# Kernel tuning notes

Hardware: AMD Instinct MI355X
Metric: run time of the kernel (lower is better)

Reference implementation:

```python
import jax, jax.numpy as jnp
import numpy as np

# ---- module hyper-params (match init_kwargs) ----
B, C_IN, C_OUT, K, H, W = 16, 128, 128, 3, 56, 56
M, G, STRIDE, RED = 2, 2, 1, 16
R = max(RED, C_IN // RED)            # GC_Attention bottleneck width = 16
MO = M * C_OUT                       # gc_att output channels
GROUPS = G * C_OUT                   # grouped 1x1 fc groups = 256
IN_PG = MO // GROUPS                 # in channels per group = M // G = 1
COUT_FC = C_OUT * C_IN * K * K       # generated weight elements per sample
OUT_PG = COUT_FC // GROUPS           # out channels per group = 576
PAD = K // 2
LN_EPS = 1e-5


def setup_inputs() -> dict:
    key = jax.random.key(0)
    ks = jax.random.split(key, 6)
    sc = 0.05
    return {
        "x": jax.random.normal(ks[0], (B, C_IN, H, W), jnp.float32),
        # GC_Attention: conv_mask (1x1, C->1)
        "w_mask": jax.random.normal(ks[1], (C_IN,), jnp.float32) * sc,
        "b_mask": jnp.zeros((), jnp.float32),
        # transform: conv1x1 C->R, LayerNorm(R), ReLU, conv1x1 R->M*out
        "w1": jax.random.normal(ks[2], (R, C_IN), jnp.float32) * sc,
        "b1": jnp.zeros((R,), jnp.float32),
        "ln_g": jnp.ones((R,), jnp.float32),
        "ln_b": jnp.zeros((R,), jnp.float32),
        "w2": jax.random.normal(ks[3], (MO, R), jnp.float32) * sc,
        "b2": jnp.zeros((MO,), jnp.float32),
        # fc: grouped 1x1 conv, groups=G*out, stored [groups, out_pg, in_pg]
        "w_fc": jax.random.normal(ks[4], (GROUPS, OUT_PG, IN_PG), jnp.float32) * sc,
        "b_fc": jnp.zeros((COUT_FC,), jnp.float32),
    }


def reference(x, w_mask, b_mask, w1, b1, ln_g, ln_b, w2, b2, w_fc, b_fc):
    b, c, h, w = x.shape
    # --- GC_Attention: global-context pooling via spatial softmax ---
    mask = jnp.einsum('bchw,c->bhw', x, w_mask) + b_mask        # [b,h,w]
    att = jax.nn.softmax(mask.reshape(b, -1), axis=-1)          # [b,hw]
    ctx = jnp.einsum('bcs,bs->bc', x.reshape(b, c, -1), att)    # [b,C]
    # bottleneck transform (1x1 convs on [b,*,1,1] == dense layers)
    t = ctx @ w1.T + b1                                          # [b,R]
    mu = t.mean(-1, keepdims=True)
    var = t.var(-1, keepdims=True)
    t = (t - mu) / jnp.sqrt(var + LN_EPS) * ln_g + ln_b          # LayerNorm over R
    t = jax.nn.relu(t)
    a = jax.nn.sigmoid(t @ w2.T + b2)                            # [b, M*out]
    # --- grouped 1x1 conv: generate per-sample conv weights ---
    xw = jnp.einsum('bgi,goi->bgo', a.reshape(b, GROUPS, IN_PG), w_fc)
    xw = xw.reshape(b, COUT_FC) + b_fc
    Wd = xw.reshape(b, C_OUT, C_IN, K, K)                        # per-sample kernels
    # --- per-sample conv2d (torch: groups=b on batch-folded input) ---
    def conv1(xi, wi):
        return jax.lax.conv_general_dilated(
            xi[None], wi, (STRIDE, STRIDE), [(PAD, PAD), (PAD, PAD)],
            dimension_numbers=('NCHW', 'OIHW', 'NCHW'))[0]
    return jax.vmap(conv1)(x, Wd)                                # [b, out, H, W]
```

## Files before the change

kernel.cpp:

```cpp
#include <hip/hip_runtime.h>
#include <hip/hip_bf16.h>
#include <math.h>

#define BATCH 16
#define CIN   128
#define COUT  128
#define SS    3136
#define XT_ROW 8192
#define XT_PER_B (58*XT_ROW)
#define NKB   18

typedef __attribute__((ext_vector_type(8))) __bf16 bf16x8;
typedef __attribute__((ext_vector_type(4))) float  floatx4;

static __device__ __forceinline__ unsigned short f2bf(float f) {
  union { float f; unsigned u; } v; v.f = f;
  unsigned r = v.u + 0x7fffu + ((v.u >> 16) & 1u);
  return (unsigned short)(r >> 16);
}
static __device__ __forceinline__ float bf2f(unsigned short u) {
  union { unsigned u; float f; } v; v.u = ((unsigned)u) << 16; return v.f;
}

static __device__ __forceinline__ float waveReduceSum(float v) {
  #pragma unroll
  for (int off = 32; off > 0; off >>= 1) v += __shfl_xor(v, off, 64);
  return v;
}

static __device__ __forceinline__ void load_lds16(const void* g, void* l) {
  __builtin_amdgcn_global_load_lds(
      (const __attribute__((address_space(1))) void*)g,
      (__attribute__((address_space(3))) void*)l, 16, 0, 0);
}

__global__ void k0_padT(const float* __restrict__ x, const float* __restrict__ w_mask,
                        const float* __restrict__ b_mask,
                        unsigned short* __restrict__ xT, float* __restrict__ rowsum,
                        float* __restrict__ pctx) {
  int b = blockIdx.y, prow = blockIdx.x, t = threadIdx.x;
  int y = prow - 1;
  __shared__ unsigned short sx[128 * 58];
  __shared__ float swm[128];
  __shared__ float red[4 * 56];
  __shared__ float se[56];
  bool rowvalid = ((unsigned)y < 56u);
  if (t < 128) swm[t] = w_mask[t];
  if (rowvalid) {
    int ci = t >> 1, h = t & 1;
    const float4* src = (const float4*)(x + (size_t)(b * 128 + ci) * SS + y * 56 + h * 28);
    #pragma unroll
    for (int c4 = 0; c4 < 7; c4++) {
      float4 v = src[c4];
      int base = ci * 58 + h * 28 + c4 * 4;
      sx[base]     = f2bf(v.x);
      sx[base + 1] = f2bf(v.y);
      sx[base + 2] = f2bf(v.z);
      sx[base + 3] = f2bf(v.w);
    }
  } else {
    for (int i = t; i < 128 * 58; i += 256) sx[i] = 0;
  }
  __syncthreads();
  if (rowvalid && t < 224) {
    int xx = t % 56, g = t / 56;
    float acc = 0.f;
    #pragma unroll
    for (int k = 0; k < 32; k++) {
      int ci = g * 32 + k;
      acc += bf2f(sx[ci * 58 + xx]) * swm[ci];
    }
    red[g * 56 + xx] = acc;
  }
  __syncthreads();
  float e = 0.f;
  if (rowvalid && t < 56) {
    float m = red[t] + red[56 + t] + red[112 + t] + red[168 + t] + b_mask[0];
    e = expf(m);
    se[t] = e;
  }
  if (t < 64) {
    float s = waveReduceSum(e);
    if (t == 0) rowsum[b * 58 + prow] = s;
  }
  __syncthreads();
  {
    int c = t >> 1, h = t & 1;
    float acc = 0.f;
    if (rowvalid) {
      #pragma unroll
      for (int j = 0; j < 28; j++)
        acc += bf2f(sx[c * 58 + h * 28 + j]) * se[h * 28 + j];
    }
    acc += __shfl_xor(acc, 1, 64);
    if (h == 0) pctx[(size_t)(b * 58 + prow) * 128 + c] = acc;
  }
  int pcol = t >> 2, cig = t & 3;
  int xx = pcol - 1;
  bool colv = rowvalid && ((unsigned)xx < 56u);
  unsigned short tmp[32];
  #pragma unroll
  for (int i = 0; i < 32; i++)
    tmp[i] = colv ? sx[(cig * 32 + i) * 58 + xx] : (unsigned short)0;
  unsigned short* dst = xT + ((size_t)(b * 58 + prow) * 64 + pcol) * 128 + cig * 32;
  #pragma unroll
  for (int q = 0; q < 4; q++)
    *reinterpret_cast<uint4*>(dst + q * 8) = *reinterpret_cast<const uint4*>(tmp + q * 8);
}

__global__ void k5_gen(const float* __restrict__ rowsum, const float* __restrict__ pctx,
                       const float* __restrict__ w1, const float* __restrict__ b1,
                       const float* __restrict__ ln_g, const float* __restrict__ ln_b,
                       const float* __restrict__ w2, const float* __restrict__ b2,
                       const float* __restrict__ w_fc, const float* __restrict__ b_fc,
                       unsigned short* __restrict__ wd) {
  int co = blockIdx.x, b = blockIdx.y, t = threadIdx.x;
  __shared__ float sc[128], st[16], sn[16], sa[2], shz;
  float rv = (t < 58) ? rowsum[b * 58 + t] : 0.f;
  float acc = 0.f;
  #pragma unroll
  for (int r = 0; r < 58; r++) acc += pctx[(size_t)(b * 58 + r) * 128 + t];
  if (t < 64) {
    float z = waveReduceSum(rv);
    if (t == 0) shz = 1.0f / z;
  }
  __syncthreads();
  sc[t] = acc * shz;
  __syncthreads();
  if (t < 16) {
    float s = b1[t];
    #pragma unroll 8
    for (int c = 0; c < 128; c++) s += sc[c] * w1[t * 128 + c];
    st[t] = s;
  }
  __syncthreads();
  float mu = 0.f, m2 = 0.f;
  #pragma unroll
  for (int r = 0; r < 16; r++) { float v = st[r]; mu += v; m2 += v * v; }
  mu *= (1.f / 16.f); m2 *= (1.f / 16.f);
  float rstd = rsqrtf(m2 - mu * mu + 1e-5f);
  if (t < 16) {
    float v = (st[t] - mu) * rstd * ln_g[t] + ln_b[t];
    sn[t] = fmaxf(v, 0.f);
  }
  __syncthreads();
  if (t < 2) {
    int mo = 2 * co + t;
    float s = b2[mo];
    #pragma unroll
    for (int r = 0; r < 16; r++) s += sn[r] * w2[mo * 16 + r];
    sa[t] = 1.f / (1.f + expf(-s));
  }
  __syncthreads();
  float a0 = sa[0], a1 = sa[1];
  const float* wrow = w_fc + co * 1152;
  const float* brow = b_fc + co * 1152;
  unsigned short* drow = wd + (size_t)(b * 128 + co) * 1152;
  #pragma unroll
  for (int r = 0; r < 9; r++) {
    int e = t + 128 * r;
    int ci = e / 9, khw = e - (e / 9) * 9;
    float v = (ci < 64 ? a0 : a1) * wrow[e] + brow[e];
    int kb = khw * 2 + (ci >> 6);
    int kq = ci & 63;
    int pos = (((kq >> 3) ^ (co & 7)) << 3) | (kq & 7);
    drow[kb * 64 + pos] = f2bf(v);
  }
}

__global__ __launch_bounds__(512, 4) void k6_conv(const unsigned short* __restrict__ xT,
                                                  const unsigned short* __restrict__ wd,
                                                  float* __restrict__ out) {
  __shared__ __align__(16) unsigned short As[8192];
  __shared__ __align__(16) unsigned short Bs[32768];
  int t = threadIdx.x;
  int b = blockIdx.y, y0 = blockIdx.x * 2;
  int wave = t >> 6, lane = t & 63, l15 = lane & 15, quad = lane >> 4;
  int x7 = lane & 7;
  const unsigned short* wp  = wd + (size_t)b * (128 * 1152);
  const unsigned short* xTb = xT + (size_t)b * XT_PER_B + (size_t)y0 * XT_ROW;

  #pragma unroll
  for (int i = 0; i < 8; i++) {
    int g = i * 512 + t;
    int row  = g >> 10;
    int pcol = (g >> 4) & 63;
    int c    = g & 15;
    int csrc = (c & 8) | ((c & 7) ^ (pcol & 7));
    load_lds16(xTb + (size_t)((row * 64 + pcol) * 16 + csrc) * 8,
               &Bs[(size_t)(i * 512 + wave * 64) * 8]);
  }

  int offA0 = (t >> 3) * 1152 + (t & 7) * 8;
  int ch1 = t + 512;
  int offA1 = (ch1 >> 3) * 1152 + (ch1 & 7) * 8;

  int s_base = (wave & 3) * 32;
  int co_b   = (wave >> 2) * 64;

  int srw[2], scl[2];
  #pragma unroll
  for (int j = 0; j < 2; j++) {
    int s = s_base + j * 16 + l15;
    int r = (s >= 56) ? 1 : 0;
    int cc = s - r * 56;
    if (s >= 112) { r = 0; cc = s - 112; }
    srw[j] = r; scl[j] = cc;
  }

  floatx4 acc[4][2];
  floatx4 zero = {0.f, 0.f, 0.f, 0.f};
  #pragma unroll
  for (int i = 0; i < 4; i++)
    #pragma unroll
    for (int j = 0; j < 2; j++) acc[i][j] = zero;

  #pragma unroll 1
  for (int kb = 0; kb < NKB; kb++) {
    int khw = kb >> 1;
    int kh = khw / 3;
    int kw = khw - kh * 3;
    __syncthreads();
    load_lds16(wp + offA0 + kb * 64, &As[wave * 512]);
    load_lds16(wp + offA1 + kb * 64, &As[4096 + wave * 512]);
    __syncthreads();
    #pragma unroll
    for (int kk = 0; kk < 2; kk++) {
      bf16x8 af[4], bfr[2];
      int pcA = ((kk * 4 + quad) ^ x7) << 3;
      #pragma unroll
      for (int i = 0; i < 4; i++)
        af[i] = *reinterpret_cast<const bf16x8*>(&As[(co_b + i * 16 + l15) * 64 + pcA]);
      int c = ((kb & 1) << 3) + kk * 4 + quad;
      #pragma unroll
      for (int j = 0; j < 2; j++) {
        int pq = scl[j] + kw;
        int cs = (c & 8) | ((c & 7) ^ (pq & 7));
        bfr[j] = *reinterpret_cast<const bf16x8*>(&Bs[(((srw[j] + kh) * 64 + pq) * 16 + cs) * 8]);
      }
      #pragma unroll
      for (int i = 0; i < 4; i++)
        #pragma unroll
        for (int j = 0; j < 2; j++)
          acc[i][j] = __builtin_amdgcn_mfma_f32_16x16x32_bf16(af[i], bfr[j], acc[i][j], 0, 0, 0);
    }
  }

  float* ob = out + (size_t)b * COUT * SS + y0 * 56;
  #pragma unroll
  for (int i = 0; i < 4; i++) {
    #pragma unroll
    for (int j = 0; j < 2; j++) {
      int sl = s_base + j * 16 + l15;
      if (sl < 112) {
        int row = (sl >= 56) ? 1 : 0;
        int col = sl - row * 56;
        #pragma unroll
        for (int r = 0; r < 4; r++) {
          int co = co_b + i * 16 + quad * 4 + r;
          ob[(size_t)co * SS + row * 56 + col] = acc[i][j][r];
        }
      }
    }
  }
}

extern "C" void kernel_launch(void* const* d_in, const int* in_sizes, int n_in,
                              void* d_out, int out_size, void* d_ws, size_t ws_size,
                              hipStream_t stream) {
  const float* x      = (const float*)d_in[0];
  const float* w_mask = (const float*)d_in[1];
  const float* b_mask = (const float*)d_in[2];
  const float* w1     = (const float*)d_in[3];
  const float* b1     = (const float*)d_in[4];
  const float* ln_g   = (const float*)d_in[5];
  const float* ln_b   = (const float*)d_in[6];
  const float* w2     = (const float*)d_in[7];
  const float* b2     = (const float*)d_in[8];
  const float* w_fc   = (const float*)d_in[9];
  const float* b_fc   = (const float*)d_in[10];
  float* out = (float*)d_out;

  char* ws = (char*)d_ws;
  unsigned short* xT  = (unsigned short*)(ws);
  unsigned short* wdw = (unsigned short*)(ws + 15204352);
  float* rowsum = (float*)(ws + 19922944);
  float* pctx   = (float*)(ws + 19927040);

  k0_padT<<<dim3(58, 16),  dim3(256), 0, stream>>>(x, w_mask, b_mask, xT, rowsum, pctx);
  k5_gen <<<dim3(128, 16), dim3(128), 0, stream>>>(rowsum, pctx, w1, b1, ln_g, ln_b,
                                                   w2, b2, w_fc, b_fc, wdw);
  k6_conv<<<dim3(28, 16),  dim3(512), 0, stream>>>(xT, wdw, out);
}
```

Baseline: 136.9 us.

## Double-buffer weight tiles and split input halo into channel halves to shrink LDS

Reorders the generated weight layout so the K loop runs over two channel halves, each with nine kernel taps. The conv kernel now stages only one 64-channel half of the padded input rows (58 columns) at a time, which cuts LDS use. It also double-buffers the weight tile with explicit vmcnt waits and barriers so the next tap's load overlaps the current MFMAs. The cost is that the input halo is loaded twice per block with an extra barrier stage, and correctness depends on hand-written waitcnt ordering.

```diff
diff --git a/kernel.cpp b/kernel.cpp
--- a/kernel.cpp
+++ b/kernel.cpp
@@ -8,7 +8,6 @@
 #define SS    3136
 #define XT_ROW 8192
 #define XT_PER_B (58*XT_ROW)
-#define NKB   18
 
 typedef __attribute__((ext_vector_type(8))) __bf16 bf16x8;
 typedef __attribute__((ext_vector_type(4))) float  floatx4;
@@ -33,6 +32,10 @@
       (const __attribute__((address_space(1))) void*)g,
       (__attribute__((address_space(3))) void*)l, 16, 0, 0);
 }
+
+#define ASM_WAIT_VM2 asm volatile("s_waitcnt vmcnt(2)" ::: "memory")
+#define ASM_WAIT_VM0 asm volatile("s_waitcnt vmcnt(0)" ::: "memory")
+#define BARRIER      __builtin_amdgcn_s_barrier()
 
 __global__ void k0_padT(const float* __restrict__ x, const float* __restrict__ w_mask,
                         const float* __restrict__ b_mask,
@@ -161,7 +164,7 @@
     int e = t + 128 * r;
     int ci = e / 9, khw = e - (e / 9) * 9;
     float v = (ci < 64 ? a0 : a1) * wrow[e] + brow[e];
-    int kb = khw * 2 + (ci >> 6);
+    int kb = (ci >> 6) * 9 + khw;
     int kq = ci & 63;
     int pos = (((kq >> 3) ^ (co & 7)) << 3) | (kq & 7);
     drow[kb * 64 + pos] = f2bf(v);
@@ -171,8 +174,8 @@
 __global__ __launch_bounds__(512, 4) void k6_conv(const unsigned short* __restrict__ xT,
                                                   const unsigned short* __restrict__ wd,
                                                   float* __restrict__ out) {
-  __shared__ __align__(16) unsigned short As[8192];
-  __shared__ __align__(16) unsigned short Bs[32768];
+  __shared__ __align__(16) unsigned short As[2][8192];
+  __shared__ __align__(16) unsigned short Bs[14848];
   int t = threadIdx.x;
   int b = blockIdx.y, y0 = blockIdx.x * 2;
   int wave = t >> 6, lane = t & 63, l15 = lane & 15, quad = lane >> 4;
@@ -180,17 +183,6 @@
   const unsigned short* wp  = wd + (size_t)b * (128 * 1152);
   const unsigned short* xTb = xT + (size_t)b * XT_PER_B + (size_t)y0 * XT_ROW;
 
-  #pragma unroll
-  for (int i = 0; i < 8; i++) {
-    int g = i * 512 + t;
-    int row  = g >> 10;
-    int pcol = (g >> 4) & 63;
-    int c    = g & 15;
-    int csrc = (c & 8) | ((c & 7) ^ (pcol & 7));
-    load_lds16(xTb + (size_t)((row * 64 + pcol) * 16 + csrc) * 8,
-               &Bs[(size_t)(i * 512 + wave * 64) * 8]);
-  }
-
   int offA0 = (t >> 3) * 1152 + (t & 7) * 8;
   int ch1 = t + 512;
   int offA1 = (ch1 >> 3) * 1152 + (ch1 & 7) * 8;
@@ -216,33 +208,55 @@
     for (int j = 0; j < 2; j++) acc[i][j] = zero;
 
   #pragma unroll 1
-  for (int kb = 0; kb < NKB; kb++) {
-    int khw = kb >> 1;
-    int kh = khw / 3;
-    int kw = khw - kh * 3;
-    __syncthreads();
-    load_lds16(wp + offA0 + kb * 64, &As[wave * 512]);
-    load_lds16(wp + offA1 + kb * 64, &As[4096 + wave * 512]);
-    __syncthreads();
-    #pragma unroll
-    for (int kk = 0; kk < 2; kk++) {
-      bf16x8 af[4], bfr[2];
-      int pcA = ((kk * 4 + quad) ^ x7) << 3;
+  for (int p = 0; p < 2; p++) {
+    #pragma unroll
+    for (int r = 0; r < 4; r++) {
+      int wc = r * 8 + wave;
+      if (wc < 29) {
+        int g = wc * 64 + lane;
+        int row = g / 464;
+        int rem = g - row * 464;
+        int pcol = rem >> 3, c = rem & 7;
+        int csrc = c ^ (pcol & 7);
+        load_lds16(xTb + (size_t)(row * 64 + pcol) * 128 + p * 64 + csrc * 8,
+                   &Bs[wc * 512]);
+      }
+    }
+    load_lds16(wp + offA0 + (p * 9) * 64, &As[0][wave * 512]);
+    load_lds16(wp + offA1 + (p * 9) * 64, &As[0][4096 + wave * 512]);
+    #pragma unroll 1
+    for (int k = 0; k < 9; k++) {
+      int P = k & 1;
+      if (k < 8) {
+        load_lds16(wp + offA0 + (p * 9 + k + 1) * 64, &As[1 - P][wave * 512]);
+        load_lds16(wp + offA1 + (p * 9 + k + 1) * 64, &As[1 - P][4096 + wave * 512]);
+        ASM_WAIT_VM2;
+      } else {
+        ASM_WAIT_VM0;
+      }
+      BARRIER;
+      int kh = k / 3, kw = k - kh * 3;
       #pragma unroll
-      for (int i = 0; i < 4; i++)
-        af[i] = *reinterpret_cast<const bf16x8*>(&As[(co_b + i * 16 + l15) * 64 + pcA]);
-      int c = ((kb & 1) << 3) + kk * 4 + quad;
-      #pragma unroll
-      for (int j = 0; j < 2; j++) {
-        int pq = scl[j] + kw;
-        int cs = (c & 8) | ((c & 7) ^ (pq & 7));
-        bfr[j] = *reinterpret_cast<const bf16x8*>(&Bs[(((srw[j] + kh) * 64 + pq) * 16 + cs) * 8]);
+      for (int kk = 0; kk < 2; kk++) {
+        bf16x8 af[4], bfr[2];
+        int pcA = ((kk * 4 + quad) ^ x7) << 3;
+        #pragma unroll
+        for (int i = 0; i < 4; i++)
+          af[i] = *reinterpret_cast<const bf16x8*>(&As[P][(co_b + i * 16 + l15) * 64 + pcA]);
+        int c = kk * 4 + quad;
+        #pragma unroll
+        for (int j = 0; j < 2; j++) {
+          int pq = scl[j] + kw;
+          bfr[j] = *reinterpret_cast<const bf16x8*>(
+              &Bs[(((srw[j] + kh) * 58 + pq) * 8 + (c ^ (pq & 7))) * 8]);
+        }
+        #pragma unroll
+        for (int i = 0; i < 4; i++)
+          #pragma unroll
+          for (int j = 0; j < 2; j++)
+            acc[i][j] = __builtin_amdgcn_mfma_f32_16x16x32_bf16(af[i], bfr[j], acc[i][j], 0, 0, 0);
       }
-      #pragma unroll
-      for (int i = 0; i < 4; i++)
-        #pragma unroll
-        for (int j = 0; j < 2; j++)
-          acc[i][j] = __builtin_amdgcn_mfma_f32_16x16x32_bf16(af[i], bfr[j], acc[i][j], 0, 0, 0);
+      BARRIER;
     }
   }
 
```

Measured after the change: 136.1 us. No clear change (-0.6%).
